# Optimization experiments

Measured on AMD Instinct MI355X. Metric: run time of the kernel, lower is better.

## Reference

```python
import jax, jax.numpy as jnp
import numpy as np

N_POINTS = 64
N_COLS = 500000
N_ANGS = N_POINTS * (N_POINTS - 1) // 2  # 2016


def setup_inputs() -> dict:
    key = jax.random.key(0)
    k1, k2 = jax.random.split(key)
    X = jax.random.normal(k1, (N_POINTS, N_COLS), dtype=jnp.float32)
    angles = 0.1 * jax.random.normal(k2, (N_ANGS,), dtype=jnp.float32)
    mus = jnp.ones((N_POINTS,), dtype=jnp.float32)
    return {"X": X, "angles": angles, "mus": mus}


def reference(X, angles, mus):
    # X: [n, m]; apply n(n-1)/2 sequential Givens rotations over row pairs
    # in order (iTop, iBtm) for iTop < iBtm, then scale rows by mus.
    # Original torch math per pair: vt' = c*vt - s*vb ; vb' = s*vt + c*vb.
    n = X.shape[0]
    top_np, btm_np = np.triu_indices(n, k=1)  # row-major order matches the double loop
    top = jnp.asarray(top_np, dtype=jnp.int32)
    btm = jnp.asarray(btm_np, dtype=jnp.int32)

    def step(Y, inp):
        a, it, ib = inp
        c = jnp.cos(a)
        s = jnp.sin(a)
        vt = Y[it]  # [m]
        vb = Y[ib]  # [m]
        Y = Y.at[it].set(c * vt - s * vb)
        Y = Y.at[ib].set(s * vt + c * vb)
        return Y, None

    Y, _ = jax.lax.scan(step, X, (angles, top, btm))
    return Y * mus[:, None]
```

## Files before the change

kernel.cpp:

```cpp
#include <hip/hip_runtime.h>
#include <hip/hip_bf16.h>

#define NPTS  64
#define NCOLS 500000
#define NANG  2016

typedef __attribute__((ext_vector_type(8))) short bf16x8;
typedef __attribute__((ext_vector_type(4))) float f32x4;

static __device__ inline short f2bf(float f) {
    union { float f; unsigned u; } uf; uf.f = f;
    unsigned u = uf.u;
    unsigned r = (u + 0x7fffu + ((u >> 16) & 1u)) >> 16;
    return (short)r;
}

static __host__ __device__ constexpr int rotS(int i) { return 63 * i - i * (i - 1) / 2; }

template<int I0, int I1>
__device__ __forceinline__ void chunk_body(const float* __restrict__ angles,
                                           float* __restrict__ P,
                                           float2* csn) {
    constexpr int K0 = rotS(I0);
    constexpr int NK = rotS(I1) - K0;
    const int tid = threadIdx.x;

    for (int t = tid; t < NK; t += 64) {
        float s, c;
        sincosf(angles[K0 + t], &s, &c);
        csn[t] = make_float2(c, s);
    }
    __syncthreads();

    float q[64 - I0];
#pragma unroll
    for (int r = I0; r < 64; ++r) q[r - I0] = (r == tid) ? 1.0f : 0.0f;

    int k = 0;
#pragma unroll
    for (int i = I0; i < I1; ++i) {
#pragma unroll
        for (int ib = i + 1; ib < 64; ++ib, ++k) {
            float c = csn[k].x, s = csn[k].y;
            float t = q[i - I0], b = q[ib - I0];
            q[ib - I0] = s * t + c * b;
            q[i - I0]  = c * t - s * b;
        }
        P[i * 64 + tid] = q[i - I0];
    }
#pragma unroll
    for (int r = 0; r < I0; ++r) P[r * 64 + tid] = (r == tid) ? 1.0f : 0.0f;
#pragma unroll
    for (int r = I1; r < 64; ++r) P[r * 64 + tid] = q[r - I0];
}

__global__ __launch_bounds__(64) void chunk_products(const float* __restrict__ angles,
                                                     float* __restrict__ ws) {
    __shared__ float2 csn[531];
    switch (blockIdx.x) {
        case 0: chunk_body< 0,  9>(angles, ws + 0 * 4096, csn); break;
        case 1: chunk_body< 9, 19>(angles, ws + 1 * 4096, csn); break;
        case 2: chunk_body<19, 32>(angles, ws + 2 * 4096, csn); break;
        default: chunk_body<32, 63>(angles, ws + 3 * 4096, csn); break;
    }
}

__global__ __launch_bounds__(256) void combine(float* __restrict__ ws,
                                               int lo_off, int hi_off, int out_off,
                                               int blk_stride,
                                               const float* __restrict__ mus) {
    const float* lo = ws + lo_off  + blockIdx.x * blk_stride;
    const float* hi = ws + hi_off  + blockIdx.x * blk_stride;
    float*      co  = ws + out_off + blockIdx.x * blk_stride;
    const int col = threadIdx.x & 63;
    const int rg  = __builtin_amdgcn_readfirstlane(threadIdx.x >> 6);

    float acc[16] = {0.f};
#pragma unroll 4
    for (int k0 = 0; k0 < 64; k0 += 4) {
        float lo0 = lo[(k0 + 0) * 64 + col];
        float lo1 = lo[(k0 + 1) * 64 + col];
        float lo2 = lo[(k0 + 2) * 64 + col];
        float lo3 = lo[(k0 + 3) * 64 + col];
#pragma unroll
        for (int r = 0; r < 16; ++r) {
            f32x4 h = *(const f32x4*)(hi + (rg * 16 + r) * 64 + k0);
            acc[r] = fmaf(h[0], lo0, acc[r]);
            acc[r] = fmaf(h[1], lo1, acc[r]);
            acc[r] = fmaf(h[2], lo2, acc[r]);
            acc[r] = fmaf(h[3], lo3, acc[r]);
        }
    }
    __syncthreads();
#pragma unroll
    for (int r = 0; r < 16; ++r) {
        float v = acc[r];
        if (mus) v *= mus[rg * 16 + r];
        co[(rg * 16 + r) * 64 + col] = v;
    }
}

__global__ __launch_bounds__(256) void apply_M(const float* __restrict__ X,
                                               const float* __restrict__ M,
                                               float* __restrict__ out,
                                               int nfull, int wstride) {
    const int lane  = threadIdx.x & 63;
    const int wave  = threadIdx.x >> 6;
    const int laneN = lane & 15;
    const int quad  = lane >> 4;

    bf16x8 afrag[4][2];
#pragma unroll
    for (int t = 0; t < 4; ++t) {
#pragma unroll
        for (int q = 0; q < 2; ++q) {
            const float* src = M + (t * 16 + laneN) * NPTS + q * 32 + quad * 8;
            bf16x8 f;
#pragma unroll
            for (int j = 0; j < 8; ++j) f[j] = f2bf(src[j]);
            afrag[t][q] = f;
        }
    }

    const int gw = blockIdx.x * 4 + wave;

    for (int s = gw; s < nfull; s += wstride) {
        const long col0 = (long)s * 64 + 4 * laneN;
        const float* xb = X + col0;

        bf16x8 bfrag[4][2];
#pragma unroll
        for (int q = 0; q < 2; ++q) {
#pragma unroll
            for (int j = 0; j < 8; ++j) {
                const int kk = q * 32 + quad * 8 + j;
                f32x4 v = *(const f32x4*)(xb + (long)kk * NCOLS);
#pragma unroll
                for (int u = 0; u < 4; ++u)
                    bfrag[u][q][j] = f2bf(v[u]);
            }
        }

#pragma unroll
        for (int t = 0; t < 4; ++t) {
            f32x4 acc[4];
#pragma unroll
            for (int u = 0; u < 4; ++u) {
                f32x4 a = {0.f, 0.f, 0.f, 0.f};
                a = __builtin_amdgcn_mfma_f32_16x16x32_bf16(afrag[t][0], bfrag[u][0], a, 0, 0, 0);
                a = __builtin_amdgcn_mfma_f32_16x16x32_bf16(afrag[t][1], bfrag[u][1], a, 0, 0, 0);
                acc[u] = a;
            }
#pragma unroll
            for (int rr = 0; rr < 4; ++rr) {
                const int row = t * 16 + quad * 4 + rr;
                f32x4 o = { acc[0][rr], acc[1][rr], acc[2][rr], acc[3][rr] };
                __builtin_nontemporal_store(o, (f32x4*)(out + (long)row * NCOLS + col0));
            }
        }
    }

    if (gw < 2) {
        const int col = nfull * 64 + gw * 16 + laneN;
        const float* xb = X + col;
        bf16x8 bfrag[2];
#pragma unroll
        for (int q = 0; q < 2; ++q) {
            bf16x8 f;
#pragma unroll
            for (int j = 0; j < 8; ++j)
                f[j] = f2bf(xb[(long)(q * 32 + quad * 8 + j) * NCOLS]);
            bfrag[q] = f;
        }
#pragma unroll
        for (int t = 0; t < 4; ++t) {
            f32x4 a = {0.f, 0.f, 0.f, 0.f};
            a = __builtin_amdgcn_mfma_f32_16x16x32_bf16(afrag[t][0], bfrag[0], a, 0, 0, 0);
            a = __builtin_amdgcn_mfma_f32_16x16x32_bf16(afrag[t][1], bfrag[1], a, 0, 0, 0);
#pragma unroll
            for (int rr = 0; rr < 4; ++rr)
                __builtin_nontemporal_store(a[rr],
                    out + (long)(t * 16 + quad * 4 + rr) * NCOLS + col);
        }
    }
}

extern "C" void kernel_launch(void* const* d_in, const int* in_sizes, int n_in,
                              void* d_out, int out_size, void* d_ws, size_t ws_size,
                              hipStream_t stream) {
    const float* X      = (const float*)d_in[0];
    const float* angles = (const float*)d_in[1];
    const float* mus    = (const float*)d_in[2];
    float* out = (float*)d_out;
    float* wsf = (float*)d_ws;

    chunk_products<<<4, 64, 0, stream>>>(angles, wsf);
    combine<<<2, 256, 0, stream>>>(wsf, 0, 4096, 0, 8192, nullptr);
    combine<<<1, 256, 0, stream>>>(wsf, 0, 2 * 4096, 4096, 0, mus);

    const int nfull  = NCOLS / 64;
    const int blocks = 1953;
    apply_M<<<blocks, 256, 0, stream>>>(X, wsf + 4096, out, nfull, blocks * 4);
}
```

Before: 276.9 us.

## Fuse rotation-matrix build and apply into one kernel with redundant per-block build

Replaces the four-kernel pipeline (chunk products, two combines, apply) with a single kernel. Every block now recomputes all 2016 sincos values and the two-chunk product of the 64x64 rotation matrix in shared memory, then applies it with MFMA. The grid shrinks from 1953 to 768 blocks so the redundant build is amortised over more columns per block. This removes three launches and the serial dependency between them. In exchange each block runs a long serial Givens chain: one wave walks 44 rows, about 1100 rotations, before the streaming work can start.

```diff
diff --git a/kernel.cpp b/kernel.cpp
--- a/kernel.cpp
+++ b/kernel.cpp
@@ -1,14 +1,16 @@
 #include <hip/hip_runtime.h>
-#include <hip/hip_bf16.h>
 
-#define NPTS  64
-#define NCOLS 500000
-#define NANG  2016
+#define NPTS   64
+#define NCOLS  500000
+#define NANG   2016
+#define NFULL  7812
+#define BLOCKS 768
+#define WSTRIDE (BLOCKS * 4)
 
 typedef __attribute__((ext_vector_type(8))) short bf16x8;
 typedef __attribute__((ext_vector_type(4))) float f32x4;
 
-static __device__ inline short f2bf(float f) {
+static __device__ __forceinline__ short f2bf(float f) {
     union { float f; unsigned u; } uf; uf.f = f;
     unsigned u = uf.u;
     unsigned r = (u + 0x7fffu + ((u >> 16) & 1u)) >> 16;
@@ -18,23 +20,11 @@
 static __host__ __device__ constexpr int rotS(int i) { return 63 * i - i * (i - 1) / 2; }
 
 template<int I0, int I1>
-__device__ __forceinline__ void chunk_body(const float* __restrict__ angles,
-                                           float* __restrict__ P,
-                                           float2* csn) {
-    constexpr int K0 = rotS(I0);
-    constexpr int NK = rotS(I1) - K0;
-    const int tid = threadIdx.x;
-
-    for (int t = tid; t < NK; t += 64) {
-        float s, c;
-        sincosf(angles[K0 + t], &s, &c);
-        csn[t] = make_float2(c, s);
-    }
-    __syncthreads();
-
+__device__ __forceinline__ void chunk_lds(const float2* __restrict__ csn,
+                                          float* __restrict__ P, int lane) {
     float q[64 - I0];
 #pragma unroll
-    for (int r = I0; r < 64; ++r) q[r - I0] = (r == tid) ? 1.0f : 0.0f;
+    for (int r = I0; r < 64; ++r) q[r - I0] = (r == lane) ? 1.0f : 0.0f;
 
     int k = 0;
 #pragma unroll
@@ -46,66 +36,60 @@
             q[ib - I0] = s * t + c * b;
             q[i - I0]  = c * t - s * b;
         }
-        P[i * 64 + tid] = q[i - I0];
+        P[i * 64 + lane] = q[i - I0];
     }
 #pragma unroll
-    for (int r = 0; r < I0; ++r) P[r * 64 + tid] = (r == tid) ? 1.0f : 0.0f;
+    for (int r = 0; r < I0; ++r) P[r * 64 + lane] = (r == lane) ? 1.0f : 0.0f;
 #pragma unroll
-    for (int r = I1; r < 64; ++r) P[r * 64 + tid] = q[r - I0];
+    for (int r = I1; r < 64; ++r) P[r * 64 + lane] = q[r - I0];
 }
 
-__global__ __launch_bounds__(64) void chunk_products(const float* __restrict__ angles,
-                                                     float* __restrict__ ws) {
-    __shared__ float2 csn[531];
-    switch (blockIdx.x) {
-        case 0: chunk_body< 0,  9>(angles, ws + 0 * 4096, csn); break;
-        case 1: chunk_body< 9, 19>(angles, ws + 1 * 4096, csn); break;
-        case 2: chunk_body<19, 32>(angles, ws + 2 * 4096, csn); break;
-        default: chunk_body<32, 63>(angles, ws + 3 * 4096, csn); break;
-    }
-}
+__global__ __launch_bounds__(256) void fused_ortho(const float* __restrict__ X,
+                                                   const float* __restrict__ angles,
+                                                   const float* __restrict__ mus,
+                                                   float* __restrict__ out) {
+    __shared__ __align__(16) float sm[12288];
+    const int tid  = threadIdx.x;
+    const int lane = tid & 63;
+    const int wave = __builtin_amdgcn_readfirstlane(tid >> 6);
 
-__global__ __launch_bounds__(256) void combine(float* __restrict__ ws,
-                                               int lo_off, int hi_off, int out_off,
-                                               int blk_stride,
-                                               const float* __restrict__ mus) {
-    const float* lo = ws + lo_off  + blockIdx.x * blk_stride;
-    const float* hi = ws + hi_off  + blockIdx.x * blk_stride;
-    float*      co  = ws + out_off + blockIdx.x * blk_stride;
-    const int col = threadIdx.x & 63;
-    const int rg  = __builtin_amdgcn_readfirstlane(threadIdx.x >> 6);
-
-    float acc[16] = {0.f};
-#pragma unroll 4
-    for (int k0 = 0; k0 < 64; k0 += 4) {
-        float lo0 = lo[(k0 + 0) * 64 + col];
-        float lo1 = lo[(k0 + 1) * 64 + col];
-        float lo2 = lo[(k0 + 2) * 64 + col];
-        float lo3 = lo[(k0 + 3) * 64 + col];
-#pragma unroll
-        for (int r = 0; r < 16; ++r) {
-            f32x4 h = *(const f32x4*)(hi + (rg * 16 + r) * 64 + k0);
-            acc[r] = fmaf(h[0], lo0, acc[r]);
-            acc[r] = fmaf(h[1], lo1, acc[r]);
-            acc[r] = fmaf(h[2], lo2, acc[r]);
-            acc[r] = fmaf(h[3], lo3, acc[r]);
-        }
+    float2* csn = (float2*)sm;
+    for (int t = tid; t < NANG; t += 256) {
+        float s, c;
+        sincosf(angles[t], &s, &c);
+        csn[t] = make_float2(c, s);
     }
     __syncthreads();
+
+    float* P0 = sm + 4096;
+    float* P1 = sm + 8192;
+    if (wave == 0)      chunk_lds<0, 19>(csn, P0, lane);
+    else if (wave == 1) chunk_lds<19, 63>(csn + rotS(19), P1, lane);
+    __syncthreads();
+
+    {
+        float acc[16] = {0.f};
+#pragma unroll 4
+        for (int k0 = 0; k0 < 64; k0 += 4) {
+            float lo0 = P0[(k0 + 0) * 64 + lane];
+            float lo1 = P0[(k0 + 1) * 64 + lane];
+            float lo2 = P0[(k0 + 2) * 64 + lane];
+            float lo3 = P0[(k0 + 3) * 64 + lane];
 #pragma unroll
-    for (int r = 0; r < 16; ++r) {
-        float v = acc[r];
-        if (mus) v *= mus[rg * 16 + r];
-        co[(rg * 16 + r) * 64 + col] = v;
+            for (int r = 0; r < 16; ++r) {
+                const f32x4 h = *(const f32x4*)&P1[(wave * 16 + r) * 64 + k0];
+                acc[r] = fmaf(h[0], lo0, acc[r]);
+                acc[r] = fmaf(h[1], lo1, acc[r]);
+                acc[r] = fmaf(h[2], lo2, acc[r]);
+                acc[r] = fmaf(h[3], lo3, acc[r]);
+            }
+        }
+#pragma unroll
+        for (int r = 0; r < 16; ++r)
+            sm[(wave * 16 + r) * 64 + lane] = acc[r] * mus[wave * 16 + r];
     }
-}
+    __syncthreads();
 
-__global__ __launch_bounds__(256) void apply_M(const float* __restrict__ X,
-                                               const float* __restrict__ M,
-                                               float* __restrict__ out,
-                                               int nfull, int wstride) {
-    const int lane  = threadIdx.x & 63;
-    const int wave  = threadIdx.x >> 6;
     const int laneN = lane & 15;
     const int quad  = lane >> 4;
 
@@ -114,7 +98,7 @@
     for (int t = 0; t < 4; ++t) {
 #pragma unroll
         for (int q = 0; q < 2; ++q) {
-            const float* src = M + (t * 16 + laneN) * NPTS + q * 32 + quad * 8;
+            const float* src = sm + (t * 16 + laneN) * 64 + q * 32 + quad * 8;
             bf16x8 f;
 #pragma unroll
             for (int j = 0; j < 8; ++j) f[j] = f2bf(src[j]);
@@ -124,7 +108,7 @@
 
     const int gw = blockIdx.x * 4 + wave;
 
-    for (int s = gw; s < nfull; s += wstride) {
+    for (int s = gw; s < NFULL; s += WSTRIDE) {
         const long col0 = (long)s * 64 + 4 * laneN;
         const float* xb = X + col0;
 
@@ -161,7 +145,7 @@
     }
 
     if (gw < 2) {
-        const int col = nfull * 64 + gw * 16 + laneN;
+        const int col = NFULL * 64 + gw * 16 + laneN;
         const float* xb = X + col;
         bf16x8 bfrag[2];
 #pragma unroll
@@ -191,14 +175,5 @@
     const float* X      = (const float*)d_in[0];
     const float* angles = (const float*)d_in[1];
     const float* mus    = (const float*)d_in[2];
-    float* out = (float*)d_out;
-    float* wsf = (float*)d_ws;
-
-    chunk_products<<<4, 64, 0, stream>>>(angles, wsf);
-    combine<<<2, 256, 0, stream>>>(wsf, 0, 4096, 0, 8192, nullptr);
-    combine<<<1, 256, 0, stream>>>(wsf, 0, 2 * 4096, 4096, 0, mus);
-
-    const int nfull  = NCOLS / 64;
-    const int blocks = 1953;
-    apply_M<<<blocks, 256, 0, stream>>>(X, wsf + 4096, out, nfull, blocks * 4);
+    fused_ortho<<<BLOCKS, 256, 0, stream>>>(X, angles, mus, (float*)d_out);
 }
```

After: 322.0 us. 1.16x slower.
